# Kernel optimization log

Hardware: AMD Instinct MI355X
Metric: run time of the kernel (lower is better)

## Reference

```python
import jax, jax.numpy as jnp
import numpy as np
import math

B, S, D, H, P = 4, 2048, 512, 8, 64
HD = D // H


def setup_inputs() -> dict:
    key = jax.random.key(0)
    ks = jax.random.split(key, 12)
    inp = {
        "query": jax.random.normal(ks[0], (B, S, D), jnp.float32),
        "key": jax.random.normal(ks[1], (B, S, D), jnp.float32),
        "value": jax.random.normal(ks[2], (B, S, D), jnp.float32),
        "query_pos_em": jax.random.normal(ks[3], (B, S, P), jnp.float32),
        "key_pos_em": jax.random.normal(ks[4], (B, S, P), jnp.float32),
        "mask": jax.random.randint(ks[5], (B, S), 0, 2, jnp.int32),
        # learned params (bias=False linears, LayerNorm affine)
        "Wq": jax.random.normal(ks[6], (D, D), jnp.float32) / math.sqrt(D),
        "Wk": jax.random.normal(ks[7], (D, D), jnp.float32) / math.sqrt(D),
        "Wv": jax.random.normal(ks[8], (D, D), jnp.float32) / math.sqrt(D),
        "Wo": jax.random.normal(ks[9], (D, D), jnp.float32) / math.sqrt(D),
        "ln_gamma": jnp.ones((D,), jnp.float32),
        "ln_beta": jnp.zeros((D,), jnp.float32),
    }
    return inp


def _split_heads(x):
    # (B,S,D) -> (B,H,S,HD)
    return x.reshape(B, S, H, HD).transpose(0, 2, 1, 3)


def reference(query, key, value, query_pos_em, key_pos_em, mask,
              Wq, Wk, Wv, Wo, ln_gamma, ln_beta):
    residual = query
    q = _split_heads(query @ Wq)
    k = _split_heads(key @ Wk)
    v = _split_heads(value @ Wv)

    # positional similarity: softmax over (B,S,S)
    simi = jax.nn.softmax(jnp.einsum('bqp,bkp->bqk', query_pos_em, key_pos_em), axis=-1)

    # scaled dot-product modulated elementwise by similarity (broadcast over heads)
    prod = jnp.einsum('bhqd,bhkd->bhqk', q, k) / math.sqrt(HD)
    prod = prod * simi[:, None, :, :]

    # additive mask: (mask-1)*1e8, broadcast [:, None, None, :]
    m = (mask.astype(prod.dtype) - 1.0) * 1e8
    prod = prod + m[:, None, None, :]

    attn = jax.nn.softmax(prod, axis=-1)
    out = jnp.einsum('bhqk,bhkd->bhqd', attn, v)  # (B,H,S,HD)
    out = out.transpose(0, 2, 1, 3).reshape(B, S, D)
    out = out @ Wo  # dropout is identity in eval mode

    x = residual + out
    mu = jnp.mean(x, axis=-1, keepdims=True)
    var = jnp.var(x, axis=-1, keepdims=True)
    return (x - mu) / jnp.sqrt(var + 1e-5) * ln_gamma + ln_beta
```

## Files before the change

kernel.cpp:

```cpp
#include <hip/hip_runtime.h>
#include <hip/hip_bf16.h>

#define Bq 4
#define Sq 2048
#define Dq 512
#define Hq 8
#define HDq 64
#define Pq 64

typedef __attribute__((ext_vector_type(8))) short short8;
typedef __attribute__((ext_vector_type(4))) float f32x4;

__device__ inline unsigned short f2bf(float f) {
  unsigned int u = __float_as_uint(f);
  unsigned int r = u + 0x7FFFu + ((u >> 16) & 1u);
  return (unsigned short)(r >> 16);
}
__device__ inline float bf2f(unsigned short s) {
  return __uint_as_float(((unsigned int)s) << 16);
}
__device__ inline short8 ld8f(const float* __restrict__ p) {
  const float4 a = *(const float4*)p;
  const float4 b = *(const float4*)(p + 4);
  short8 r;
  r[0] = (short)f2bf(a.x); r[1] = (short)f2bf(a.y); r[2] = (short)f2bf(a.z); r[3] = (short)f2bf(a.w);
  r[4] = (short)f2bf(b.x); r[5] = (short)f2bf(b.y); r[6] = (short)f2bf(b.z); r[7] = (short)f2bf(b.w);
  return r;
}

__global__ __launch_bounds__(256) void prep(const float* __restrict__ qpe,
                                            const float* __restrict__ kpe,
                                            const int* __restrict__ mask,
                                            unsigned short* __restrict__ qpeb,
                                            unsigned short* __restrict__ kpeb,
                                            float* __restrict__ mb) {
  const int bid = blockIdx.x;
  if (bid < 256) {
    int i = bid * 256 + threadIdx.x;
    *(short8*)&qpeb[(size_t)i * 8] = ld8f(qpe + (size_t)i * 8);
  } else if (bid < 512) {
    int i = (bid - 256) * 256 + threadIdx.x;
    *(short8*)&kpeb[(size_t)i * 8] = ld8f(kpe + (size_t)i * 8);
  } else {
    int i = (bid - 512) * 256 + threadIdx.x;
    mb[i] = ((float)mask[i] - 1.0f) * 1.442695041e8f;
  }
}

__global__ __launch_bounds__(256) void convW4(const float* __restrict__ Wq,
                                              const float* __restrict__ Wk,
                                              const float* __restrict__ Wv,
                                              const float* __restrict__ Wo,
                                              unsigned short* __restrict__ Wqt,
                                              unsigned short* __restrict__ Wkt,
                                              unsigned short* __restrict__ Wvt,
                                              unsigned short* __restrict__ Wot) {
  __shared__ float tile[32][33];
  const int z = blockIdx.z;
  const float* W = z == 0 ? Wq : z == 1 ? Wk : z == 2 ? Wv : Wo;
  unsigned short* Wt = z == 0 ? Wqt : z == 1 ? Wkt : z == 2 ? Wvt : Wot;
  const float scale = (z == 0) ? 0.125f : 1.0f;
  const int tx = threadIdx.x & 31, ty = threadIdx.x >> 5;
  const int n0 = blockIdx.x * 32, k0 = blockIdx.y * 32;
  for (int j = 0; j < 4; ++j)
    tile[ty + j * 8][tx] = W[(size_t)(k0 + ty + j * 8) * Dq + n0 + tx];
  __syncthreads();
  for (int j = 0; j < 4; ++j)
    Wt[(size_t)(n0 + ty + j * 8) * Dq + k0 + tx] = f2bf(tile[tx][ty + j * 8] * scale);
}

__global__ __launch_bounds__(256) void gemm_qkv(const float* __restrict__ Aq,
                                                const float* __restrict__ Ak,
                                                const float* __restrict__ Av,
                                                const unsigned short* __restrict__ Wqt,
                                                const unsigned short* __restrict__ Wkt,
                                                const unsigned short* __restrict__ Wvt,
                                                unsigned short* __restrict__ Qb,
                                                unsigned short* __restrict__ Kb,
                                                unsigned short* __restrict__ VbT) {
  __shared__ unsigned short Alds[128][72];
  __shared__ unsigned short Blds[128][72];
  const int z = blockIdx.z;
  const float* Ap = z == 0 ? Aq : z == 1 ? Ak : Av;
  const unsigned short* Wt = z == 0 ? Wqt : z == 1 ? Wkt : Wvt;
  unsigned short* Cb = z == 0 ? Qb : z == 1 ? Kb : VbT;
  const bool wt = (z == 2);
  const int tid = threadIdx.x;
  const int lane = tid & 63, wv = tid >> 6;
  const int wr = wv >> 1, wc = wv & 1;
  const int l15 = lane & 15, lg = lane >> 4;
  const int row0 = blockIdx.x * 128, col0 = blockIdx.y * 128;
  f32x4 acc[4][4] = {};
  for (int k0 = 0; k0 < Dq; k0 += 64) {
    __syncthreads();
#pragma unroll
    for (int j = 0; j < 4; ++j) {
      int s = tid + j * 256;
      int r = s >> 3, c8 = (s & 7) * 8;
      const float* ap = Ap + (size_t)(row0 + r) * Dq + k0 + c8;
      float4 f0 = *(const float4*)ap;
      float4 f1 = *(const float4*)(ap + 4);
      short8 u;
      u[0] = (short)f2bf(f0.x); u[1] = (short)f2bf(f0.y);
      u[2] = (short)f2bf(f0.z); u[3] = (short)f2bf(f0.w);
      u[4] = (short)f2bf(f1.x); u[5] = (short)f2bf(f1.y);
      u[6] = (short)f2bf(f1.z); u[7] = (short)f2bf(f1.w);
      *(short8*)&Alds[r][c8] = u;
      *(uint4*)&Blds[r][c8] = *(const uint4*)&Wt[(size_t)(col0 + r) * Dq + k0 + c8];
    }
    __syncthreads();
#pragma unroll
    for (int kc = 0; kc < 2; ++kc) {
      short8 a[4], b[4];
#pragma unroll
      for (int mi = 0; mi < 4; ++mi)
        a[mi] = *(const short8*)&Alds[wr * 64 + mi * 16 + l15][kc * 32 + lg * 8];
#pragma unroll
      for (int ni = 0; ni < 4; ++ni)
        b[ni] = *(const short8*)&Blds[wc * 64 + ni * 16 + l15][kc * 32 + lg * 8];
#pragma unroll
      for (int mi = 0; mi < 4; ++mi)
#pragma unroll
        for (int ni = 0; ni < 4; ++ni)
          acc[mi][ni] = __builtin_amdgcn_mfma_f32_16x16x32_bf16(a[mi], b[ni], acc[mi][ni], 0, 0, 0);
    }
  }
  const int orow = row0 + wr * 64 + lg * 4;
  const int ocol = col0 + wc * 64 + l15;
  if (wt) {
    const int bidx = orow >> 11;
#pragma unroll
    for (int mi = 0; mi < 4; ++mi)
#pragma unroll
      for (int ni = 0; ni < 4; ++ni) {
        int gc = ocol + ni * 16;
        int s = (orow + mi * 16) & (Sq - 1);
        ushort4 w = {f2bf(acc[mi][ni][0]), f2bf(acc[mi][ni][1]),
                     f2bf(acc[mi][ni][2]), f2bf(acc[mi][ni][3])};
        *(ushort4*)&Cb[((size_t)(bidx * Dq + gc)) * Sq + s] = w;
      }
  } else {
#pragma unroll
    for (int mi = 0; mi < 4; ++mi)
#pragma unroll
      for (int ni = 0; ni < 4; ++ni)
#pragma unroll
        for (int rr = 0; rr < 4; ++rr) {
          int gr = orow + mi * 16 + rr, gc = ocol + ni * 16;
          Cb[(size_t)gr * Dq + gc] = f2bf(acc[mi][ni][rr]);
        }
  }
}

__global__ __launch_bounds__(256) void gemm_wo(const unsigned short* __restrict__ Ab,
                                               const unsigned short* __restrict__ Wt,
                                               const float* __restrict__ res,
                                               float* __restrict__ Cf) {
  __shared__ unsigned short Alds[128][72];
  __shared__ unsigned short Blds[128][72];
  const int tid = threadIdx.x;
  const int lane = tid & 63, wv = tid >> 6;
  const int wr = wv >> 1, wc = wv & 1;
  const int l15 = lane & 15, lg = lane >> 4;
  const int row0 = blockIdx.x * 128, col0 = blockIdx.y * 128;
  f32x4 acc[4][4] = {};
  for (int k0 = 0; k0 < Dq; k0 += 64) {
    __syncthreads();
#pragma unroll
    for (int j = 0; j < 4; ++j) {
      int s = tid + j * 256;
      int r = s >> 3, c8 = (s & 7) * 8;
      *(uint4*)&Alds[r][c8] = *(const uint4*)&Ab[(size_t)(row0 + r) * Dq + k0 + c8];
      *(uint4*)&Blds[r][c8] = *(const uint4*)&Wt[(size_t)(col0 + r) * Dq + k0 + c8];
    }
    __syncthreads();
#pragma unroll
    for (int kc = 0; kc < 2; ++kc) {
      short8 a[4], b[4];
#pragma unroll
      for (int mi = 0; mi < 4; ++mi)
        a[mi] = *(const short8*)&Alds[wr * 64 + mi * 16 + l15][kc * 32 + lg * 8];
#pragma unroll
      for (int ni = 0; ni < 4; ++ni)
        b[ni] = *(const short8*)&Blds[wc * 64 + ni * 16 + l15][kc * 32 + lg * 8];
#pragma unroll
      for (int mi = 0; mi < 4; ++mi)
#pragma unroll
        for (int ni = 0; ni < 4; ++ni)
          acc[mi][ni] = __builtin_amdgcn_mfma_f32_16x16x32_bf16(a[mi], b[ni], acc[mi][ni], 0, 0, 0);
    }
  }
  const int orow = row0 + wr * 64 + lg * 4;
  const int ocol = col0 + wc * 64 + l15;
#pragma unroll
  for (int mi = 0; mi < 4; ++mi)
#pragma unroll
    for (int ni = 0; ni < 4; ++ni)
#pragma unroll
      for (int rr = 0; rr < 4; ++rr) {
        int gr = orow + mi * 16 + rr, gc = ocol + ni * 16;
        Cf[(size_t)gr * Dq + gc] = acc[mi][ni][rr] + res[(size_t)gr * Dq + gc];
      }
}

__global__ __launch_bounds__(256) void possim(const unsigned short* __restrict__ qpe,
                                              const unsigned short* __restrict__ kpe,
                                              unsigned short* __restrict__ simiB,
                                              float* __restrict__ invsum) {
  __shared__ float wsum[4][16];
  const int tid = threadIdx.x, lane = tid & 63, wv = tid >> 6;
  const int l15 = lane & 15, lg = lane >> 4;
  const int b = blockIdx.y, q0 = blockIdx.x * 16;
  const unsigned short* qrow = qpe + ((size_t)(b * Sq + q0 + l15)) * Pq + lg * 8;
  short8 aq0 = *(const short8*)qrow;
  short8 aq1 = *(const short8*)(qrow + 32);
  unsigned short* sB = simiB + ((size_t)(b * (Sq / 16) + blockIdx.x)) * Sq * 16;
  float lsum[4] = {0.f, 0.f, 0.f, 0.f};
  for (int t = wv; t < Sq / 64; t += 4) {
    int k0 = t * 64;
    f32x4 sc[4] = {};
#pragma unroll
    for (int ng = 0; ng < 4; ++ng) {
      const unsigned short* krow = kpe + ((size_t)(b * Sq + k0 + ng * 16 + l15)) * Pq + lg * 8;
      short8 bk0 = *(const short8*)krow;
      short8 bk1 = *(const short8*)(krow + 32);
      sc[ng] = __builtin_amdgcn_mfma_f32_16x16x32_bf16(aq0, bk0, sc[ng], 0, 0, 0);
      sc[ng] = __builtin_amdgcn_mfma_f32_16x16x32_bf16(aq1, bk1, sc[ng], 0, 0, 0);
    }
#pragma unroll
    for (int ng = 0; ng < 4; ++ng) {
      float e0 = __expf(sc[ng][0]);
      float e1 = __expf(sc[ng][1]);
      float e2 = __expf(sc[ng][2]);
      float e3 = __expf(sc[ng][3]);
      lsum[0] += e0; lsum[1] += e1; lsum[2] += e2; lsum[3] += e3;
      ushort4 st = {f2bf(e0), f2bf(e1), f2bf(e2), f2bf(e3)};
      *(ushort4*)&sB[(size_t)(k0 + ng * 16 + l15) * 16 + lg * 4] = st;
    }
  }
  for (int rr = 0; rr < 4; ++rr)
    for (int m = 1; m < 16; m <<= 1) lsum[rr] += __shfl_xor(lsum[rr], m, 64);
  if (l15 == 0)
    for (int rr = 0; rr < 4; ++rr) wsum[wv][lg * 4 + rr] = lsum[rr];
  __syncthreads();
  if (tid < 16) {
    float tot = wsum[0][tid] + wsum[1][tid] + wsum[2][tid] + wsum[3][tid];
    invsum[b * Sq + q0 + tid] = 1.0f / tot;
  }
}

__global__ __launch_bounds__(512) void attn(const unsigned short* __restrict__ Qb,
                                            const unsigned short* __restrict__ Kb,
                                            const unsigned short* __restrict__ VbT,
                                            const unsigned short* __restrict__ simiB,
                                            const float* __restrict__ invsum,
                                            const float* __restrict__ mbias,
                                            unsigned short* __restrict__ O) {
  __shared__ unsigned short Klds[2][64][72];
  __shared__ unsigned short Vlds[2][64][72];
  __shared__ unsigned short Plds[8][16][72];
  const int tid = threadIdx.x, lane = tid & 63, wv = tid >> 6;
  const int l15 = lane & 15, lg = lane >> 4;
  const int q0 = blockIdx.x * 128, h = blockIdx.y, b = blockIdx.z;
  const int qw = q0 + wv * 16;
  const int sr = tid >> 3, sc8 = (tid & 7) * 8;
  const unsigned short* Kg = Kb + ((size_t)(b * Sq + sr)) * Dq + h * HDq + sc8;
  const unsigned short* Vg = VbT + ((size_t)(b * Dq + h * HDq + sr)) * Sq + sc8;

  const unsigned short* qp = Qb + ((size_t)(b * Sq + qw + l15)) * Dq + h * HDq + lg * 8;
  short8 aq0 = *(const short8*)qp;
  short8 aq1 = *(const short8*)(qp + 32);
  float inv2[4];
#pragma unroll
  for (int rr = 0; rr < 4; ++rr)
    inv2[rr] = invsum[b * Sq + qw + lg * 4 + rr] * 1.442695041f;
  const unsigned short* sB =
      simiB + ((size_t)(b * (Sq / 16) + blockIdx.x * 8 + wv)) * Sq * 16 + lg * 4;
  const float* Mb = mbias + b * Sq;
  const int wxor = (lg >> 1) << 3;
  const int lgs = lg ^ (l15 >> 3);

  {
    *(uint4*)&Klds[0][sr][sc8] = *(const uint4*)Kg;
    *(uint4*)&Vlds[0][sr][sc8] = *(const uint4*)Vg;
  }
  f32x4 oacc[4] = {};
  float lsum[4] = {0.f, 0.f, 0.f, 0.f};
  int cur = 0;
  for (int t = 0; t < Sq / 64; ++t) {
    const int k0 = t * 64;
    __syncthreads();
    uint4 nk0, nv0;
    const bool more = (t < Sq / 64 - 1);
    if (more) {
      nk0 = *(const uint4*)(Kg + (size_t)(k0 + 64) * Dq);
      nv0 = *(const uint4*)(Vg + (k0 + 64));
    }
    ushort4 sv4[4];
    float mbf[4];
#pragma unroll
    for (int ng = 0; ng < 4; ++ng) {
      int kk = k0 + ng * 16 + l15;
      sv4[ng] = *(const ushort4*)&sB[(size_t)kk * 16];
      mbf[ng] = Mb[kk];
    }
    f32x4 sc[4] = {};
    __builtin_amdgcn_s_setprio(1);
#pragma unroll
    for (int ng = 0; ng < 4; ++ng) {
      short8 bk0 = *(const short8*)&Klds[cur][ng * 16 + l15][lg * 8];
      short8 bk1 = *(const short8*)&Klds[cur][ng * 16 + l15][32 + lg * 8];
      sc[ng] = __builtin_amdgcn_mfma_f32_16x16x32_bf16(aq0, bk0, sc[ng], 0, 0, 0);
      sc[ng] = __builtin_amdgcn_mfma_f32_16x16x32_bf16(aq1, bk1, sc[ng], 0, 0, 0);
    }
    __builtin_amdgcn_s_setprio(0);
#pragma unroll
    for (int ng = 0; ng < 4; ++ng) {
#pragma unroll
      for (int rr = 0; rr < 4; ++rr) {
        float sv = bf2f(rr == 0 ? sv4[ng].x : rr == 1 ? sv4[ng].y : rr == 2 ? sv4[ng].z
                                                                            : sv4[ng].w);
        float p = __builtin_amdgcn_exp2f(fmaf(sc[ng][rr] * sv, inv2[rr], mbf[ng]));
        lsum[rr] += p;
        Plds[wv][lg * 4 + rr][ng * 16 + (l15 ^ wxor)] = f2bf(p);
      }
    }
    short8 pa0 = *(const short8*)&Plds[wv][l15][lgs * 8];
    short8 pa1 = *(const short8*)&Plds[wv][l15][32 + lgs * 8];
    __builtin_amdgcn_s_setprio(1);
#pragma unroll
    for (int dg = 0; dg < 4; ++dg) {
      short8 bv0 = *(const short8*)&Vlds[cur][dg * 16 + l15][lg * 8];
      short8 bv1 = *(const short8*)&Vlds[cur][dg * 16 + l15][32 + lg * 8];
      oacc[dg] = __builtin_amdgcn_mfma_f32_16x16x32_bf16(pa0, bv0, oacc[dg], 0, 0, 0);
      oacc[dg] = __builtin_amdgcn_mfma_f32_16x16x32_bf16(pa1, bv1, oacc[dg], 0, 0, 0);
    }
    __builtin_amdgcn_s_setprio(0);
    if (more) {
      *(uint4*)&Klds[cur ^ 1][sr][sc8] = nk0;
      *(uint4*)&Vlds[cur ^ 1][sr][sc8] = nv0;
      cur ^= 1;
    }
  }
#pragma unroll
  for (int rr = 0; rr < 4; ++rr)
    for (int m = 1; m < 16; m <<= 1) lsum[rr] += __shfl_xor(lsum[rr], m, 64);
#pragma unroll
  for (int dg = 0; dg < 4; ++dg)
    for (int rr = 0; rr < 4; ++rr) {
      int qg = qw + lg * 4 + rr;
      O[((size_t)(b * Sq + qg)) * Dq + h * HDq + dg * 16 + l15] = f2bf(oacc[dg][rr] / lsum[rr]);
    }
}

__global__ __launch_bounds__(256) void lnorm(float* __restrict__ X,
                                             const float* __restrict__ gamma,
                                             const float* __restrict__ beta) {
  const int tid = threadIdx.x, lane = tid & 63, wv = tid >> 6;
  const int row = blockIdx.x * 4 + wv;
  float* xr = X + (size_t)row * Dq + lane * 8;
  float4 x0 = *(float4*)xr;
  float4 x1 = *(float4*)(xr + 4);
  float s = x0.x + x0.y + x0.z + x0.w + x1.x + x1.y + x1.z + x1.w;
  float s2 = x0.x * x0.x + x0.y * x0.y + x0.z * x0.z + x0.w * x0.w +
             x1.x * x1.x + x1.y * x1.y + x1.z * x1.z + x1.w * x1.w;
  for (int m = 1; m < 64; m <<= 1) {
    s += __shfl_xor(s, m, 64);
    s2 += __shfl_xor(s2, m, 64);
  }
  float mu = s * (1.0f / 512.0f);
  float var = s2 * (1.0f / 512.0f) - mu * mu;
  float rstd = rsqrtf(var + 1e-5f);
  const float* g = gamma + lane * 8;
  const float* be = beta + lane * 8;
  float4 y0, y1;
  y0.x = (x0.x - mu) * rstd * g[0] + be[0];
  y0.y = (x0.y - mu) * rstd * g[1] + be[1];
  y0.z = (x0.z - mu) * rstd * g[2] + be[2];
  y0.w = (x0.w - mu) * rstd * g[3] + be[3];
  y1.x = (x1.x - mu) * rstd * g[4] + be[4];
  y1.y = (x1.y - mu) * rstd * g[5] + be[5];
  y1.z = (x1.z - mu) * rstd * g[6] + be[6];
  y1.w = (x1.w - mu) * rstd * g[7] + be[7];
  *(float4*)xr = y0;
  *(float4*)(xr + 4) = y1;
}

extern "C" void kernel_launch(void* const* d_in, const int* in_sizes, int n_in,
                              void* d_out, int out_size, void* d_ws, size_t ws_size,
                              hipStream_t stream) {
  const float* query = (const float*)d_in[0];
  const float* key = (const float*)d_in[1];
  const float* value = (const float*)d_in[2];
  const float* qpe = (const float*)d_in[3];
  const float* kpe = (const float*)d_in[4];
  const int* mask = (const int*)d_in[5];
  const float* Wq = (const float*)d_in[6];
  const float* Wk = (const float*)d_in[7];
  const float* Wv = (const float*)d_in[8];
  const float* Wo = (const float*)d_in[9];
  const float* gamma = (const float*)d_in[10];
  const float* beta = (const float*)d_in[11];
  float* out = (float*)d_out;

  char* ws = (char*)d_ws;
  size_t off = 0;
  unsigned short* Qb = (unsigned short*)(ws + off); off += (size_t)Bq * Sq * Dq * 2;
  unsigned short* Kb = (unsigned short*)(ws + off); off += (size_t)Bq * Sq * Dq * 2;
  unsigned short* VbT = (unsigned short*)(ws + off); off += (size_t)Bq * Sq * Dq * 2;
  unsigned short* Wqt = (unsigned short*)(ws + off); off += (size_t)Dq * Dq * 2;
  unsigned short* Wkt = (unsigned short*)(ws + off); off += (size_t)Dq * Dq * 2;
  unsigned short* Wvt = (unsigned short*)(ws + off); off += (size_t)Dq * Dq * 2;
  unsigned short* Wot = (unsigned short*)(ws + off); off += (size_t)Dq * Dq * 2;
  unsigned short* simiB = (unsigned short*)(ws + off); off += (size_t)Bq * Sq * Sq * 2;
  float* invsum = (float*)(ws + off); off += (size_t)Bq * Sq * 4;
  float* mbias = (float*)(ws + off); off += (size_t)Bq * Sq * 4;
  unsigned short* Ob = (unsigned short*)(ws + off); off += (size_t)Bq * Sq * Dq * 2;
  unsigned short* qpeb = (unsigned short*)(ws + off); off += (size_t)Bq * Sq * Pq * 2;
  unsigned short* kpeb = (unsigned short*)(ws + off); off += (size_t)Bq * Sq * Pq * 2;

  dim3 blk(256);
  prep<<<dim3(544), blk, 0, stream>>>(qpe, kpe, mask, qpeb, kpeb, mbias);
  convW4<<<dim3(16, 16, 4), blk, 0, stream>>>(Wq, Wk, Wv, Wo, Wqt, Wkt, Wvt, Wot);
  possim<<<dim3(Sq / 16, Bq), blk, 0, stream>>>(qpeb, kpeb, simiB, invsum);
  gemm_qkv<<<dim3(64, 4, 3), blk, 0, stream>>>(query, key, value, Wqt, Wkt, Wvt, Qb, Kb, VbT);
  attn<<<dim3(Sq / 128, Hq, Bq), dim3(512), 0, stream>>>(Qb, Kb, VbT, simiB, invsum, mbias, Ob);
  gemm_wo<<<dim3(64, 4), blk, 0, stream>>>(Ob, Wot, query, out);
  lnorm<<<dim3(Bq * Sq / 4), blk, 0, stream>>>(out, gamma, beta);
}
```

Baseline: 149.1 us.

## Merge prep and weight conversion kernels, prefetch simi/mask, drop P swizzle

Merges the input-prep and weight-transpose/convert kernels into one launch, saving one kernel launch and its gap. In the attention loop, the positional-similarity and mask-bias loads for the next key tile are now issued alongside the K/V prefetch, hiding their global latency behind the current tile's compute at the cost of extra registers. It also removes the XOR swizzle on the P tile in LDS, which simplifies indexing but may bring back bank conflicts on the P writes and reads.

Result: no change. 148.6 us (-0.3%).

```diff
diff --git a/kernel.cpp b/kernel.cpp
--- a/kernel.cpp
+++ b/kernel.cpp
@@ -28,12 +28,21 @@
   return r;
 }
 
-__global__ __launch_bounds__(256) void prep(const float* __restrict__ qpe,
-                                            const float* __restrict__ kpe,
-                                            const int* __restrict__ mask,
-                                            unsigned short* __restrict__ qpeb,
-                                            unsigned short* __restrict__ kpeb,
-                                            float* __restrict__ mb) {
+__global__ __launch_bounds__(256) void prep_conv(const float* __restrict__ qpe,
+                                                 const float* __restrict__ kpe,
+                                                 const int* __restrict__ mask,
+                                                 const float* __restrict__ Wq,
+                                                 const float* __restrict__ Wk,
+                                                 const float* __restrict__ Wv,
+                                                 const float* __restrict__ Wo,
+                                                 unsigned short* __restrict__ qpeb,
+                                                 unsigned short* __restrict__ kpeb,
+                                                 float* __restrict__ mb,
+                                                 unsigned short* __restrict__ Wqt,
+                                                 unsigned short* __restrict__ Wkt,
+                                                 unsigned short* __restrict__ Wvt,
+                                                 unsigned short* __restrict__ Wot) {
+  __shared__ float tile[32][33];
   const int bid = blockIdx.x;
   if (bid < 256) {
     int i = bid * 256 + threadIdx.x;
@@ -41,32 +50,23 @@
   } else if (bid < 512) {
     int i = (bid - 256) * 256 + threadIdx.x;
     *(short8*)&kpeb[(size_t)i * 8] = ld8f(kpe + (size_t)i * 8);
-  } else {
+  } else if (bid < 544) {
     int i = (bid - 512) * 256 + threadIdx.x;
     mb[i] = ((float)mask[i] - 1.0f) * 1.442695041e8f;
-  }
-}
-
-__global__ __launch_bounds__(256) void convW4(const float* __restrict__ Wq,
-                                              const float* __restrict__ Wk,
-                                              const float* __restrict__ Wv,
-                                              const float* __restrict__ Wo,
-                                              unsigned short* __restrict__ Wqt,
-                                              unsigned short* __restrict__ Wkt,
-                                              unsigned short* __restrict__ Wvt,
-                                              unsigned short* __restrict__ Wot) {
-  __shared__ float tile[32][33];
-  const int z = blockIdx.z;
-  const float* W = z == 0 ? Wq : z == 1 ? Wk : z == 2 ? Wv : Wo;
-  unsigned short* Wt = z == 0 ? Wqt : z == 1 ? Wkt : z == 2 ? Wvt : Wot;
-  const float scale = (z == 0) ? 0.125f : 1.0f;
-  const int tx = threadIdx.x & 31, ty = threadIdx.x >> 5;
-  const int n0 = blockIdx.x * 32, k0 = blockIdx.y * 32;
-  for (int j = 0; j < 4; ++j)
-    tile[ty + j * 8][tx] = W[(size_t)(k0 + ty + j * 8) * Dq + n0 + tx];
-  __syncthreads();
-  for (int j = 0; j < 4; ++j)
-    Wt[(size_t)(n0 + ty + j * 8) * Dq + k0 + tx] = f2bf(tile[tx][ty + j * 8] * scale);
+  } else {
+    const int cid = bid - 544;
+    const int x = cid & 15, y = (cid >> 4) & 15, z = cid >> 8;
+    const float* W = z == 0 ? Wq : z == 1 ? Wk : z == 2 ? Wv : Wo;
+    unsigned short* Wt = z == 0 ? Wqt : z == 1 ? Wkt : z == 2 ? Wvt : Wot;
+    const float scale = (z == 0) ? 0.125f : 1.0f;
+    const int tx = threadIdx.x & 31, ty = threadIdx.x >> 5;
+    const int n0 = x * 32, k0 = y * 32;
+    for (int j = 0; j < 4; ++j)
+      tile[ty + j * 8][tx] = W[(size_t)(k0 + ty + j * 8) * Dq + n0 + tx];
+    __syncthreads();
+    for (int j = 0; j < 4; ++j)
+      Wt[(size_t)(n0 + ty + j * 8) * Dq + k0 + tx] = f2bf(tile[tx][ty + j * 8] * scale);
+  }
 }
 
 __global__ __launch_bounds__(256) void gemm_qkv(const float* __restrict__ Aq,
@@ -277,9 +277,15 @@
   const unsigned short* sB =
       simiB + ((size_t)(b * (Sq / 16) + blockIdx.x * 8 + wv)) * Sq * 16 + lg * 4;
   const float* Mb = mbias + b * Sq;
-  const int wxor = (lg >> 1) << 3;
-  const int lgs = lg ^ (l15 >> 3);
-
+
+  ushort4 sv4[4];
+  float mbf[4];
+#pragma unroll
+  for (int ng = 0; ng < 4; ++ng) {
+    int kk = ng * 16 + l15;
+    sv4[ng] = *(const ushort4*)&sB[(size_t)kk * 16];
+    mbf[ng] = Mb[kk];
+  }
   {
     *(uint4*)&Klds[0][sr][sc8] = *(const uint4*)Kg;
     *(uint4*)&Vlds[0][sr][sc8] = *(const uint4*)Vg;
@@ -291,18 +297,18 @@
     const int k0 = t * 64;
     __syncthreads();
     uint4 nk0, nv0;
+    ushort4 nsv[4];
+    float nmb[4];
     const bool more = (t < Sq / 64 - 1);
     if (more) {
       nk0 = *(const uint4*)(Kg + (size_t)(k0 + 64) * Dq);
       nv0 = *(const uint4*)(Vg + (k0 + 64));
-    }
-    ushort4 sv4[4];
-    float mbf[4];
-#pragma unroll
-    for (int ng = 0; ng < 4; ++ng) {
-      int kk = k0 + ng * 16 + l15;
-      sv4[ng] = *(const ushort4*)&sB[(size_t)kk * 16];
-      mbf[ng] = Mb[kk];
+#pragma unroll
+      for (int ng = 0; ng < 4; ++ng) {
+        int kk = k0 + 64 + ng * 16 + l15;
+        nsv[ng] = *(const ushort4*)&sB[(size_t)kk * 16];
+        nmb[ng] = Mb[kk];
+      }
     }
     f32x4 sc[4] = {};
     __builtin_amdgcn_s_setprio(1);
@@ -322,11 +328,11 @@
                                                                             : sv4[ng].w);
         float p = __builtin_amdgcn_exp2f(fmaf(sc[ng][rr] * sv, inv2[rr], mbf[ng]));
         lsum[rr] += p;
-        Plds[wv][lg * 4 + rr][ng * 16 + (l15 ^ wxor)] = f2bf(p);
+        Plds[wv][lg * 4 + rr][ng * 16 + l15] = f2bf(p);
       }
     }
-    short8 pa0 = *(const short8*)&Plds[wv][l15][lgs * 8];
-    short8 pa1 = *(const short8*)&Plds[wv][l15][32 + lgs * 8];
+    short8 pa0 = *(const short8*)&Plds[wv][l15][lg * 8];
+    short8 pa1 = *(const short8*)&Plds[wv][l15][32 + lg * 8];
     __builtin_amdgcn_s_setprio(1);
 #pragma unroll
     for (int dg = 0; dg < 4; ++dg) {
@@ -339,6 +345,11 @@
     if (more) {
       *(uint4*)&Klds[cur ^ 1][sr][sc8] = nk0;
       *(uint4*)&Vlds[cur ^ 1][sr][sc8] = nv0;
+#pragma unroll
+      for (int ng = 0; ng < 4; ++ng) {
+        sv4[ng] = nsv[ng];
+        mbf[ng] = nmb[ng];
+      }
       cur ^= 1;
     }
   }
@@ -420,8 +431,8 @@
   unsigned short* kpeb = (unsigned short*)(ws + off); off += (size_t)Bq * Sq * Pq * 2;
 
   dim3 blk(256);
-  prep<<<dim3(544), blk, 0, stream>>>(qpe, kpe, mask, qpeb, kpeb, mbias);
-  convW4<<<dim3(16, 16, 4), blk, 0, stream>>>(Wq, Wk, Wv, Wo, Wqt, Wkt, Wvt, Wot);
+  prep_conv<<<dim3(544 + 1024), blk, 0, stream>>>(qpe, kpe, mask, Wq, Wk, Wv, Wo, qpeb, kpeb,
+                                                  mbias, Wqt, Wkt, Wvt, Wot);
   possim<<<dim3(Sq / 16, Bq), blk, 0, stream>>>(qpeb, kpeb, simiB, invsum);
   gemm_qkv<<<dim3(64, 4, 3), blk, 0, stream>>>(query, key, value, Wqt, Wkt, Wvt, Qb, Kb, VbT);
   attn<<<dim3(Sq / 128, Hq, Bq), dim3(512), 0, stream>>>(Qb, Kb, VbT, simiB, invsum, mbias, Ob);
```
